# Kernel tuning notes

Measured on AMD Instinct MI355X. Metric: run time of the kernel, lower is better.

The kernel has to match this reference:

```python
import jax, jax.numpy as jnp
import numpy as np

B, S, D, H = 4, 2048, 1024, 16
HD = D // H  # 64
EPS = 1e-6


def _layernorm(x, scale, bias):
    mu = jnp.mean(x, axis=-1, keepdims=True)
    var = jnp.mean(jnp.square(x - mu), axis=-1, keepdims=True)
    return (x - mu) * jax.lax.rsqrt(var + EPS) * scale + bias


def setup_inputs() -> dict:
    key = jax.random.key(0)
    ks = jax.random.split(key, 10)
    s = 0.02
    return {
        "x": jax.random.normal(ks[0], (B, S, D), jnp.float32),
        "attention_mask": jnp.ones((B, 1, S, S), jnp.bool_),
        "eval": 1,
        "Wq": jax.random.normal(ks[1], (D, D), jnp.float32) * s,
        "bq": jnp.zeros((D,), jnp.float32),
        "Wk": jax.random.normal(ks[2], (D, D), jnp.float32) * s,
        "bk": jnp.zeros((D,), jnp.float32),
        "Wv": jax.random.normal(ks[3], (D, D), jnp.float32) * s,
        "bv": jnp.zeros((D,), jnp.float32),
        "Wo": jax.random.normal(ks[4], (D, D), jnp.float32) * s,
        "bo": jnp.zeros((D,), jnp.float32),
        "W1": jax.random.normal(ks[5], (D, D), jnp.float32) * s,
        "b1": jnp.zeros((D,), jnp.float32),
        "W2": jax.random.normal(ks[6], (D, D), jnp.float32) * s,
        "b2": jnp.zeros((D,), jnp.float32),
        "ln1_scale": jnp.ones((D,), jnp.float32),
        "ln1_bias": jnp.zeros((D,), jnp.float32),
        "ln2_scale": jnp.ones((D,), jnp.float32),
        "ln2_bias": jnp.zeros((D,), jnp.float32),
    }


def reference(x, attention_mask, eval, Wq, bq, Wk, bk, Wv, bv, Wo, bo,
              W1, b1, W2, b2, ln1_scale, ln1_bias, ln2_scale, ln2_bias):
    # --- MultiHeadAttention ---
    q = (x @ Wq + bq).reshape(B, S, H, HD)
    k = (x @ Wk + bk).reshape(B, S, H, HD)
    v = (x @ Wv + bv).reshape(B, S, H, HD)
    scores = jnp.einsum('bqhd,bkhd->bhqk', q, k) / jnp.sqrt(jnp.float32(HD))
    scores = jnp.where(attention_mask, scores, -jnp.inf)
    attn = jax.nn.softmax(scores, axis=-1)
    vals = jnp.einsum('bhqk,bkhd->bqhd', attn, v).reshape(B, S, D)
    attn_out = vals @ Wo + bo
    # --- residual + LN ---
    h = _layernorm(x + attn_out, ln1_scale, ln1_bias)
    # --- FeedForward (dropout deterministic -> identity) ---
    ff = jnp.maximum(h @ W1 + b1, 0.0) @ W2 + b2
    return _layernorm(h + ff, ln2_scale, ln2_bias)
```

## Files before the change

### kernel.cpp

```cpp
#include <hip/hip_runtime.h>

typedef __bf16 bf16;
typedef __bf16 bf16x8 __attribute__((ext_vector_type(8)));
typedef __bf16 bf16x4 __attribute__((ext_vector_type(4)));
typedef float f32x4 __attribute__((ext_vector_type(4)));
typedef float f32x16 __attribute__((ext_vector_type(16)));
typedef unsigned int uint;

#define BB 4
#define SS 2048
#define DD 1024
#define HH 16
#define HD 64
#define GM 8192
#define GN 1024
#define GK 1024
#define KVB 64
#define NT (SS / KVB)

__device__ __forceinline__ f32x4 mfma16(bf16x8 a, bf16x8 b, f32x4 c) {
    return __builtin_amdgcn_mfma_f32_16x16x32_bf16(a, b, c, 0, 0, 0);
}
__device__ __forceinline__ f32x16 mfma32(bf16x8 a, bf16x8 b, f32x16 c) {
    return __builtin_amdgcn_mfma_f32_32x32x16_bf16(a, b, c, 0, 0, 0);
}
__device__ __forceinline__ uint pack2(float x, float y) {
    union { bf16 b[2]; uint u; } uu;
    uu.b[0] = (bf16)x; uu.b[1] = (bf16)y;
    return uu.u;
}
__device__ __forceinline__ void gload16(const bf16* g, char* l) {
    __builtin_amdgcn_global_load_lds((const __attribute__((address_space(1))) void*)g,
                                     (__attribute__((address_space(3))) void*)l, 16, 0, 0);
}

__global__ __launch_bounds__(256) void cvt_kernel(const float* __restrict__ in, bf16* __restrict__ out, int n4) {
    int i = blockIdx.x * 256 + threadIdx.x;
    if (i < n4) {
        float4 v = *(const float4*)(in + (size_t)i * 4);
        bf16x4 o = {(bf16)v.x, (bf16)v.y, (bf16)v.z, (bf16)v.w};
        *(bf16x4*)(out + (size_t)i * 4) = o;
    }
}

__global__ __launch_bounds__(256) void wtrans6_kernel(const float* __restrict__ Wa, const float* __restrict__ Wb,
                                                      const float* __restrict__ Wc, const float* __restrict__ Wd,
                                                      const float* __restrict__ We, const float* __restrict__ Wf,
                                                      bf16* __restrict__ WtBase) {
    __shared__ float tile[64][65];
    const int t = threadIdx.x;
    const int z = blockIdx.z;
    const float* W = (z == 0) ? Wa : (z == 1) ? Wb : (z == 2) ? Wc : (z == 3) ? Wd : (z == 4) ? We : Wf;
    bf16* Wt = WtBase + ((size_t)z << 20);
    const int k0 = blockIdx.x * 64, n0 = blockIdx.y * 64;
#pragma unroll
    for (int i = 0; i < 16; ++i) {
        int idx = i * 256 + t;
        int r = idx >> 6, c = idx & 63;
        tile[r][c] = W[(size_t)(k0 + r) * DD + n0 + c];
    }
    __syncthreads();
#pragma unroll
    for (int i = 0; i < 16; ++i) {
        int idx = i * 256 + t;
        int r = idx >> 6, c = idx & 63;
        Wt[(size_t)(n0 + r) * DD + k0 + c] = (bf16)tile[c][r];
    }
}

__global__ __launch_bounds__(256) void vtrans_kernel(const bf16* __restrict__ V, bf16* __restrict__ Vt) {
    __shared__ bf16 tile[64][72];
    const int t = threadIdx.x;
    const int bh = blockIdx.y;
    const int b = bh >> 4, h = bh & 15;
    const int s0 = blockIdx.x * 64;
#pragma unroll
    for (int i = 0; i < 16; ++i) {
        int idx = i * 256 + t;
        int r = idx >> 6, c = idx & 63;
        tile[r][c] = V[(size_t)(b * SS + s0 + r) * DD + h * HD + c];
    }
    __syncthreads();
#pragma unroll
    for (int i = 0; i < 16; ++i) {
        int idx = i * 256 + t;
        int r = idx >> 6, c = idx & 63;
        Vt[((size_t)bh * HD + r) * SS + s0 + c] = tile[c][r];
    }
}

#define STAGE(buf, kt) { const int off_ = (kt) * 32; \
    gload16(pa + off_, lpa + (buf) * 16384); \
    gload16(pb + off_, lpb + (buf) * 16384); }

#define WAITB(n) { asm volatile("s_waitcnt vmcnt(" #n ")" ::: "memory"); \
    __builtin_amdgcn_s_barrier(); \
    __builtin_amdgcn_sched_barrier(0); }

#define KSTEP(c) { \
    const char* Asc_ = smem + (c) * 16384; \
    const char* Bsc_ = Asc_ + 8192; \
    bf16x8 af[2], bfr[4]; \
    _Pragma("unroll") for (int mi = 0; mi < 2; ++mi) \
        af[mi] = *(const bf16x8*)(Asc_ + (wr * 32 + mi * 16 + l16) * 64 + g * 16); \
    _Pragma("unroll") for (int ni = 0; ni < 4; ++ni) \
        bfr[ni] = *(const bf16x8*)(Bsc_ + (wc * 64 + ni * 16 + l16) * 64 + g * 16); \
    _Pragma("unroll") for (int mi = 0; mi < 2; ++mi) \
        _Pragma("unroll") for (int ni = 0; ni < 4; ++ni) \
            acc[mi][ni] = mfma16(af[mi], bfr[ni], acc[mi][ni]); }

template<int MODE>
__global__ __launch_bounds__(512) void gemm_bt(const bf16* __restrict__ A, const bf16* __restrict__ Bt,
                                               const float* __restrict__ bias0, const float* __restrict__ bias1,
                                               const float* __restrict__ bias2, const float* __restrict__ resid,
                                               void* __restrict__ C0, void* __restrict__ C1, void* __restrict__ C2) {
    const int gx = gridDim.x, gy = gridDim.y;
    const int wg = blockIdx.x + gx * blockIdx.y;
    const int xcd = wg & 7, j = wg >> 3;
    const int m_blk = xcd * (gx >> 3) + j / gy;
    const int n_blk = j % gy;
    const int m0 = m_blk * 128;
    const int n0 = n_blk * 128;
    const int t = threadIdx.x;
    const int l = t & 63, wid = t >> 6;
    const int l16 = l & 15, g = l >> 4;
    const int wr = wid >> 1, wc = wid & 1;

    __shared__ char smem[65536];

    const bf16* pa = A + (size_t)(m0 + (t >> 2)) * GK + (t & 3) * 8;
    const bf16* pb = Bt + (size_t)(n0 + (t >> 2)) * GK + (t & 3) * 8;
    char* lpa = smem + t * 16;
    char* lpb = smem + 8192 + t * 16;

    f32x4 z = {0.f, 0.f, 0.f, 0.f};
    f32x4 acc[2][4];
#pragma unroll
    for (int mi = 0; mi < 2; ++mi)
#pragma unroll
        for (int ni = 0; ni < 4; ++ni) acc[mi][ni] = z;

    STAGE(0, 0) STAGE(1, 1) STAGE(2, 2)

    for (int kb = 0; kb < 28; kb += 4) {
        WAITB(4) STAGE(3, kb + 3) KSTEP(0)
        WAITB(4) STAGE(0, kb + 4) KSTEP(1)
        WAITB(4) STAGE(1, kb + 5) KSTEP(2)
        WAITB(4) STAGE(2, kb + 6) KSTEP(3)
    }
    WAITB(4) STAGE(3, 31) KSTEP(0)
    WAITB(4) KSTEP(1)
    WAITB(2) KSTEP(2)
    WAITB(0) KSTEP(3)

    const int creg = (MODE == 0) ? (n0 >> 10) : 0;
    const float* bias = (creg == 0) ? bias0 : (creg == 1) ? bias1 : bias2;
    bf16* outb = (bf16*)((creg == 0) ? C0 : (creg == 1) ? C1 : C2);
    float* outf = (float*)C0;
    const int ncol0 = (MODE == 0) ? (n0 & 1023) : n0;
#pragma unroll
    for (int ni = 0; ni < 4; ++ni) {
        const int col = ncol0 + wc * 64 + ni * 16 + l16;
        const float bv = bias[col];
#pragma unroll
        for (int mi = 0; mi < 2; ++mi) {
            const int row0 = m0 + wr * 32 + mi * 16 + g * 4;
#pragma unroll
            for (int j2 = 0; j2 < 4; ++j2) {
                float v = acc[mi][ni][j2] + bv;
                if (MODE == 2) v = fmaxf(v, 0.f);
                if (MODE == 1) {
                    v += resid[(size_t)(row0 + j2) * GN + col];
                    outf[(size_t)(row0 + j2) * GN + col] = v;
                } else {
                    outb[(size_t)(row0 + j2) * GN + col] = (bf16)v;
                }
            }
        }
    }
}

#define PFRAG(P, OFF, DST) { \
    uint a0 = pack2(P[OFF + 0], P[OFF + 1]); \
    uint a1 = pack2(P[OFF + 2], P[OFF + 3]); \
    uint a2 = pack2(P[OFF + 4], P[OFF + 5]); \
    uint a3 = pack2(P[OFF + 6], P[OFF + 7]); \
    uint s0 = (uint)__shfl_xor((int)a0, 32); \
    uint s1 = (uint)__shfl_xor((int)a1, 32); \
    uint s2 = (uint)__shfl_xor((int)a2, 32); \
    uint s3 = (uint)__shfl_xor((int)a3, 32); \
    union { uint u[4]; bf16x8 v; } uu; \
    uu.u[0] = lh ? s2 : a0; \
    uu.u[1] = lh ? s3 : a1; \
    uu.u[2] = lh ? a2 : s0; \
    uu.u[3] = lh ? a3 : s1; \
    DST = uu.v; }

__global__ __launch_bounds__(512) void attn_kernel(const bf16* __restrict__ Q, const bf16* __restrict__ K,
                                                   const bf16* __restrict__ Vt, bf16* __restrict__ vals) {
    const int wg = blockIdx.x;
    const int bh = wg >> 3;
    const int b = bh >> 4, h = bh & 15;
    const int q0 = (wg & 7) << 8;
    const int t = threadIdx.x;
    const int w = t >> 6, l = t & 63;
    const int l31 = l & 31, lh = l >> 5;
    const int qrow = q0 + w * 32 + l31;

    __shared__ int4 lds4[2048];
    char* lds = (char*)lds4;

    const float QS = 0.125f * 1.44269504f;
    const bf16* qp = Q + ((size_t)(b * SS + qrow)) * DD + h * HD + lh * 8;
    bf16x8 qf[4];
#pragma unroll
    for (int dc = 0; dc < 4; ++dc) {
        bf16x8 v = *(const bf16x8*)(qp + dc * 16);
#pragma unroll
        for (int j = 0; j < 8; ++j) v[j] = (bf16)((float)v[j] * QS);
        qf[dc] = v;
    }

    const int srow = t >> 3, schunk = t & 7;
    const bf16* kgp = K + ((size_t)(b * SS + srow)) * DD + h * HD + schunk * 8;
    const bf16* vgp = Vt + ((size_t)(bh * HD + srow)) * SS + schunk * 8;
    const int soff = srow * 128 + ((schunk * 16) ^ ((srow & 7) << 4));

    int4 rk = *(const int4*)kgp;
    int4 rv = *(const int4*)vgp;
    *(int4*)(lds + soff) = rk;
    *(int4*)(lds + 8192 + soff) = rv;

    const int sw = (l & 7) << 4;
    f32x16 o0, o1;
#pragma unroll
    for (int i = 0; i < 16; ++i) { o0[i] = 0.f; o1[i] = 0.f; }
    float l_run = 0.f;
    __syncthreads();

    for (int kt = 0; kt < NT; ++kt) {
        const int cur = (kt & 1) << 14;
        if (kt + 1 < NT) {
            rk = *(const int4*)(kgp + (size_t)(kt + 1) * KVB * DD);
            rv = *(const int4*)(vgp + (kt + 1) * KVB);
        }
        const char* kb = lds + cur;
        const char* vb = kb + 8192;
        f32x16 st0, st1;
#pragma unroll
        for (int i = 0; i < 16; ++i) { st0[i] = 0.f; st1[i] = 0.f; }
        __builtin_amdgcn_s_setprio(1);
#pragma unroll
        for (int dc = 0; dc < 4; ++dc) {
            const int cb = (dc * 32 + lh * 16) ^ sw;
            bf16x8 ka0 = *(const bf16x8*)(kb + l31 * 128 + cb);
            bf16x8 ka1 = *(const bf16x8*)(kb + (32 + l31) * 128 + cb);
            st0 = mfma32(ka0, qf[dc], st0);
            st1 = mfma32(ka1, qf[dc], st1);
        }
        __builtin_amdgcn_s_setprio(0);
        float sum = 0.f;
#pragma unroll
        for (int i = 0; i < 16; ++i) { st0[i] = __builtin_amdgcn_exp2f(st0[i]); sum += st0[i]; }
#pragma unroll
        for (int i = 0; i < 16; ++i) { st1[i] = __builtin_amdgcn_exp2f(st1[i]); sum += st1[i]; }
        sum += __shfl_xor(sum, 32);
        l_run += sum;
        bf16x8 pf0, pf1, pf2, pf3;
        PFRAG(st0, 0, pf0); PFRAG(st0, 8, pf1); PFRAG(st1, 0, pf2); PFRAG(st1, 8, pf3);
        __builtin_amdgcn_s_setprio(1);
#pragma unroll
        for (int dt = 0; dt < 2; ++dt) {
            const int rb = (dt * 32 + l31) * 128;
            f32x16 acc = dt ? o1 : o0;
            acc = mfma32(*(const bf16x8*)(vb + rb + ((0 * 32 + lh * 16) ^ sw)), pf0, acc);
            acc = mfma32(*(const bf16x8*)(vb + rb + ((1 * 32 + lh * 16) ^ sw)), pf1, acc);
            acc = mfma32(*(const bf16x8*)(vb + rb + ((2 * 32 + lh * 16) ^ sw)), pf2, acc);
            acc = mfma32(*(const bf16x8*)(vb + rb + ((3 * 32 + lh * 16) ^ sw)), pf3, acc);
            if (dt) o1 = acc; else o0 = acc;
        }
        __builtin_amdgcn_s_setprio(0);
        if (kt + 1 < NT) {
            const int nxt = (~kt & 1) << 14;
            *(int4*)(lds + nxt + soff) = rk;
            *(int4*)(lds + nxt + 8192 + soff) = rv;
        }
        __syncthreads();
    }
    const float invl = 1.f / l_run;
    bf16* vp = vals + ((size_t)(b * SS + qrow)) * DD + h * HD;
#pragma unroll
    for (int dt = 0; dt < 2; ++dt) {
        const f32x16 oo = dt ? o1 : o0;
#pragma unroll
        for (int rg = 0; rg < 4; ++rg) {
            bf16x4 ov;
#pragma unroll
            for (int j = 0; j < 4; ++j) ov[j] = (bf16)(oo[rg * 4 + j] * invl);
            *(bf16x4*)(vp + dt * 32 + rg * 8 + lh * 4) = ov;
        }
    }
}

template<bool WB>
__global__ __launch_bounds__(256) void ln_kernel(const float* __restrict__ in,
                                                 const float* __restrict__ scale, const float* __restrict__ bias,
                                                 float* __restrict__ outf, bf16* __restrict__ outb) {
    const int row = blockIdx.x;
    const int t = threadIdx.x;
    const size_t base = (size_t)row * DD + t * 4;
    const float4 va = *(const float4*)(in + base);
    const float r0 = va.x, r1 = va.y, r2 = va.z, r3 = va.w;
    float s = r0 + r1 + r2 + r3;
    float q = r0 * r0 + r1 * r1 + r2 * r2 + r3 * r3;
#pragma unroll
    for (int d = 1; d < 64; d <<= 1) { s += __shfl_xor(s, d); q += __shfl_xor(q, d); }
    __shared__ float ss[4], qq[4];
    const int wid = t >> 6, l = t & 63;
    if (l == 0) { ss[wid] = s; qq[wid] = q; }
    __syncthreads();
    s = ss[0] + ss[1] + ss[2] + ss[3];
    q = qq[0] + qq[1] + qq[2] + qq[3];
    const float mean = s * (1.f / 1024.f);
    const float var = q * (1.f / 1024.f) - mean * mean;
    const float rstd = rsqrtf(var + 1e-6f);
    const float4 sc = *(const float4*)(scale + t * 4);
    const float4 bi = *(const float4*)(bias + t * 4);
    const float y0 = (r0 - mean) * rstd * sc.x + bi.x;
    const float y1 = (r1 - mean) * rstd * sc.y + bi.y;
    const float y2 = (r2 - mean) * rstd * sc.z + bi.z;
    const float y3 = (r3 - mean) * rstd * sc.w + bi.w;
    float4 yo; yo.x = y0; yo.y = y1; yo.z = y2; yo.w = y3;
    *(float4*)(outf + base) = yo;
    if (WB) {
        bf16x4 ob = {(bf16)y0, (bf16)y1, (bf16)y2, (bf16)y3};
        *(bf16x4*)(outb + base) = ob;
    }
}

extern "C" void kernel_launch(void* const* d_in, const int* in_sizes, int n_in,
                              void* d_out, int out_size, void* d_ws, size_t ws_size,
                              hipStream_t stream) {
    const float* x   = (const float*)d_in[0];
    const float* Wq  = (const float*)d_in[3];  const float* bq = (const float*)d_in[4];
    const float* Wk  = (const float*)d_in[5];  const float* bk = (const float*)d_in[6];
    const float* Wv  = (const float*)d_in[7];  const float* bv = (const float*)d_in[8];
    const float* Wo  = (const float*)d_in[9];  const float* bo = (const float*)d_in[10];
    const float* W1  = (const float*)d_in[11]; const float* b1 = (const float*)d_in[12];
    const float* W2  = (const float*)d_in[13]; const float* b2 = (const float*)d_in[14];
    const float* l1s = (const float*)d_in[15]; const float* l1b = (const float*)d_in[16];
    const float* l2s = (const float*)d_in[17]; const float* l2b = (const float*)d_in[18];

    char* ws = (char*)d_ws;
    bf16* WTq = (bf16*)ws;
    bf16* WTo = WTq + 3 * (1 << 20);
    bf16* WT1 = WTq + 4 * (1 << 20);
    bf16* WT2 = WTq + 5 * (1 << 20);
    char* A1 = ws + 12582912;
    char* A2 = A1 + 16777216;
    char* A3 = A2 + 16777216;
    char* A4 = A3 + 16777216;
    char* A5 = A4 + 16777216;

    bf16*  xb      = (bf16*)A1;
    bf16*  Qb      = (bf16*)A2;
    bf16*  Kb      = (bf16*)A3;
    bf16*  Vb      = (bf16*)A4;
    bf16*  Vt      = (bf16*)A5;
    bf16*  valsb   = (bf16*)A4;
    float* attnout = (float*)A2;
    float* h       = (float*)A5;
    bf16*  hb      = (bf16*)A4;
    bf16*  ff1b    = (bf16*)A1;
    float* ff2     = (float*)A2;
    float* out     = (float*)d_out;

    const dim3 blk(256);
    const dim3 gblk(512);

    wtrans6_kernel<<<dim3(16, 16, 6), blk, 0, stream>>>(Wq, Wk, Wv, Wo, W1, W2, WTq);
    cvt_kernel<<<8192, blk, 0, stream>>>(x, xb, GM * DD / 4);
    gemm_bt<0><<<dim3(GM / 128, 24), gblk, 0, stream>>>(xb, WTq, bq, bk, bv, nullptr, Qb, Kb, Vb);
    vtrans_kernel<<<dim3(SS / 64, BB * HH), blk, 0, stream>>>(Vb, Vt);
    attn_kernel<<<BB * HH * (SS / 256), 512, 0, stream>>>(Qb, Kb, Vt, valsb);
    gemm_bt<1><<<dim3(GM / 128, 8), gblk, 0, stream>>>(valsb, WTo, bo, bo, bo, x, attnout, nullptr, nullptr);
    ln_kernel<true><<<GM, blk, 0, stream>>>(attnout, l1s, l1b, h, hb);
    gemm_bt<2><<<dim3(GM / 128, 8), gblk, 0, stream>>>(hb, WT1, b1, b1, b1, nullptr, ff1b, nullptr, nullptr);
    gemm_bt<1><<<dim3(GM / 128, 8), gblk, 0, stream>>>(ff1b, WT2, b2, b2, b2, h, ff2, nullptr, nullptr);
    ln_kernel<false><<<GM, blk, 0, stream>>>(ff2, l2s, l2b, out, nullptr);
}
```

Measured before the change: 425.2 us.

## Rework GEMM to 256 threads with 32x32 MFMA, XOR-swizzled LDS and 3-stage pipeline

The GEMM kernel now uses 4 waves per 128x128 tile instead of 8. Each wave computes a 64x64 sub-tile with 32x32x16 bf16 MFMAs in place of 16x16x32. LDS rows are XOR-swizzled by chunk to cut bank conflicts, and the pipeline depth drops from four buffers to three so shared memory shrinks to 48KB. The aim is higher MFMA density and register reuse per wave, at the cost of fewer waves per block to hide latency and more loads issued per thread.

```diff
diff --git a/kernel.cpp b/kernel.cpp
--- a/kernel.cpp
+++ b/kernel.cpp
@@ -91,7 +91,9 @@
 
 #define STAGE(buf, kt) { const int off_ = (kt) * 32; \
     gload16(pa + off_, lpa + (buf) * 16384); \
-    gload16(pb + off_, lpb + (buf) * 16384); }
+    gload16(pa + 64 * GK + off_, lpa + (buf) * 16384 + 4096); \
+    gload16(pb + off_, lpb + (buf) * 16384); \
+    gload16(pb + 64 * GK + off_, lpb + (buf) * 16384 + 4096); }
 
 #define WAITB(n) { asm volatile("s_waitcnt vmcnt(" #n ")" ::: "memory"); \
     __builtin_amdgcn_s_barrier(); \
@@ -100,17 +102,18 @@
 #define KSTEP(c) { \
     const char* Asc_ = smem + (c) * 16384; \
     const char* Bsc_ = Asc_ + 8192; \
-    bf16x8 af[2], bfr[4]; \
+    bf16x8 af[2][2], bfr[2][2]; \
     _Pragma("unroll") for (int mi = 0; mi < 2; ++mi) \
-        af[mi] = *(const bf16x8*)(Asc_ + (wr * 32 + mi * 16 + l16) * 64 + g * 16); \
-    _Pragma("unroll") for (int ni = 0; ni < 4; ++ni) \
-        bfr[ni] = *(const bf16x8*)(Bsc_ + (wc * 64 + ni * 16 + l16) * 64 + g * 16); \
+      _Pragma("unroll") for (int ks = 0; ks < 2; ++ks) { \
+        af[mi][ks]  = *(const bf16x8*)(Asc_ + (wr * 64 + mi * 32 + l31) * 64 + ((ks * 32 + lh * 16) ^ sw4)); \
+        bfr[mi][ks] = *(const bf16x8*)(Bsc_ + (wc * 64 + mi * 32 + l31) * 64 + ((ks * 32 + lh * 16) ^ sw4)); } \
     _Pragma("unroll") for (int mi = 0; mi < 2; ++mi) \
-        _Pragma("unroll") for (int ni = 0; ni < 4; ++ni) \
-            acc[mi][ni] = mfma16(af[mi], bfr[ni], acc[mi][ni]); }
+      _Pragma("unroll") for (int ni = 0; ni < 2; ++ni) { \
+        acc[mi][ni] = mfma32(af[mi][0], bfr[ni][0], acc[mi][ni]); \
+        acc[mi][ni] = mfma32(af[mi][1], bfr[ni][1], acc[mi][ni]); } }
 
 template<int MODE>
-__global__ __launch_bounds__(512) void gemm_bt(const bf16* __restrict__ A, const bf16* __restrict__ Bt,
+__global__ __launch_bounds__(256) void gemm_bt(const bf16* __restrict__ A, const bf16* __restrict__ Bt,
                                                const float* __restrict__ bias0, const float* __restrict__ bias1,
                                                const float* __restrict__ bias2, const float* __restrict__ resid,
                                                void* __restrict__ C0, void* __restrict__ C1, void* __restrict__ C2) {
@@ -123,35 +126,39 @@
     const int n0 = n_blk * 128;
     const int t = threadIdx.x;
     const int l = t & 63, wid = t >> 6;
-    const int l16 = l & 15, g = l >> 4;
+    const int l31 = l & 31, lh = l >> 5;
+    const int sw4 = (l31 & 3) << 4;
     const int wr = wid >> 1, wc = wid & 1;
 
-    __shared__ char smem[65536];
-
-    const bf16* pa = A + (size_t)(m0 + (t >> 2)) * GK + (t & 3) * 8;
-    const bf16* pb = Bt + (size_t)(n0 + (t >> 2)) * GK + (t & 3) * 8;
+    __shared__ char smem[49152];
+
+    const int srow = t >> 2;
+    const int schk = (t & 3) ^ (srow & 3);
+    const bf16* pa = A + (size_t)(m0 + srow) * GK + schk * 8;
+    const bf16* pb = Bt + (size_t)(n0 + srow) * GK + schk * 8;
     char* lpa = smem + t * 16;
     char* lpb = smem + 8192 + t * 16;
 
-    f32x4 z = {0.f, 0.f, 0.f, 0.f};
-    f32x4 acc[2][4];
+    f32x16 acc[2][2];
 #pragma unroll
     for (int mi = 0; mi < 2; ++mi)
 #pragma unroll
-        for (int ni = 0; ni < 4; ++ni) acc[mi][ni] = z;
-
-    STAGE(0, 0) STAGE(1, 1) STAGE(2, 2)
-
-    for (int kb = 0; kb < 28; kb += 4) {
-        WAITB(4) STAGE(3, kb + 3) KSTEP(0)
-        WAITB(4) STAGE(0, kb + 4) KSTEP(1)
-        WAITB(4) STAGE(1, kb + 5) KSTEP(2)
-        WAITB(4) STAGE(2, kb + 6) KSTEP(3)
-    }
-    WAITB(4) STAGE(3, 31) KSTEP(0)
-    WAITB(4) KSTEP(1)
-    WAITB(2) KSTEP(2)
-    WAITB(0) KSTEP(3)
+        for (int ni = 0; ni < 2; ++ni)
+#pragma unroll
+            for (int i = 0; i < 16; ++i) acc[mi][ni][i] = 0.f;
+
+    STAGE(0, 0) STAGE(1, 1)
+
+    for (int kb = 0; kb < 27; kb += 3) {
+        WAITB(4) STAGE(2, kb + 2) KSTEP(0)
+        WAITB(4) STAGE(0, kb + 3) KSTEP(1)
+        WAITB(4) STAGE(1, kb + 4) KSTEP(2)
+    }
+    WAITB(4) STAGE(2, 29) KSTEP(0)
+    WAITB(4) STAGE(0, 30) KSTEP(1)
+    WAITB(4) STAGE(1, 31) KSTEP(2)
+    WAITB(4) KSTEP(0)
+    WAITB(0) KSTEP(1)
 
     const int creg = (MODE == 0) ? (n0 >> 10) : 0;
     const float* bias = (creg == 0) ? bias0 : (creg == 1) ? bias1 : bias2;
@@ -159,22 +166,23 @@
     float* outf = (float*)C0;
     const int ncol0 = (MODE == 0) ? (n0 & 1023) : n0;
 #pragma unroll
-    for (int ni = 0; ni < 4; ++ni) {
-        const int col = ncol0 + wc * 64 + ni * 16 + l16;
+    for (int mi = 0; mi < 2; ++mi)
+#pragma unroll
+    for (int ni = 0; ni < 2; ++ni) {
+        const int col = ncol0 + wc * 64 + ni * 32 + l31;
         const float bv = bias[col];
 #pragma unroll
-        for (int mi = 0; mi < 2; ++mi) {
-            const int row0 = m0 + wr * 32 + mi * 16 + g * 4;
-#pragma unroll
-            for (int j2 = 0; j2 < 4; ++j2) {
-                float v = acc[mi][ni][j2] + bv;
-                if (MODE == 2) v = fmaxf(v, 0.f);
-                if (MODE == 1) {
-                    v += resid[(size_t)(row0 + j2) * GN + col];
-                    outf[(size_t)(row0 + j2) * GN + col] = v;
-                } else {
-                    outb[(size_t)(row0 + j2) * GN + col] = (bf16)v;
-                }
+        for (int rg = 0; rg < 4; ++rg)
+#pragma unroll
+        for (int rr = 0; rr < 4; ++rr) {
+            const int row = m0 + wr * 64 + mi * 32 + rg * 8 + lh * 4 + rr;
+            float v = acc[mi][ni][rg * 4 + rr] + bv;
+            if (MODE == 2) v = fmaxf(v, 0.f);
+            if (MODE == 1) {
+                v += resid[(size_t)row * GN + col];
+                outf[(size_t)row * GN + col] = v;
+            } else {
+                outb[(size_t)row * GN + col] = (bf16)v;
             }
         }
     }
@@ -376,16 +384,15 @@
     float* out     = (float*)d_out;
 
     const dim3 blk(256);
-    const dim3 gblk(512);
 
     wtrans6_kernel<<<dim3(16, 16, 6), blk, 0, stream>>>(Wq, Wk, Wv, Wo, W1, W2, WTq);
     cvt_kernel<<<8192, blk, 0, stream>>>(x, xb, GM * DD / 4);
-    gemm_bt<0><<<dim3(GM / 128, 24), gblk, 0, stream>>>(xb, WTq, bq, bk, bv, nullptr, Qb, Kb, Vb);
+    gemm_bt<0><<<dim3(GM / 128, 24), blk, 0, stream>>>(xb, WTq, bq, bk, bv, nullptr, Qb, Kb, Vb);
     vtrans_kernel<<<dim3(SS / 64, BB * HH), blk, 0, stream>>>(Vb, Vt);
     attn_kernel<<<BB * HH * (SS / 256), 512, 0, stream>>>(Qb, Kb, Vt, valsb);
-    gemm_bt<1><<<dim3(GM / 128, 8), gblk, 0, stream>>>(valsb, WTo, bo, bo, bo, x, attnout, nullptr, nullptr);
+    gemm_bt<1><<<dim3(GM / 128, 8), blk, 0, stream>>>(valsb, WTo, bo, bo, bo, x, attnout, nullptr, nullptr);
     ln_kernel<true><<<GM, blk, 0, stream>>>(attnout, l1s, l1b, h, hb);
-    gemm_bt<2><<<dim3(GM / 128, 8), gblk, 0, stream>>>(hb, WT1, b1, b1, b1, nullptr, ff1b, nullptr, nullptr);
-    gemm_bt<1><<<dim3(GM / 128, 8), gblk, 0, stream>>>(ff1b, WT2, b2, b2, b2, h, ff2, nullptr, nullptr);
+    gemm_bt<2><<<dim3(GM / 128, 8), blk, 0, stream>>>(hb, WT1, b1, b1, b1, nullptr, ff1b, nullptr, nullptr);
+    gemm_bt<1><<<dim3(GM / 128, 8), blk, 0, stream>>>(ff1b, WT2, b2, b2, b2, h, ff2, nullptr, nullptr);
     ln_kernel<false><<<GM, blk, 0, stream>>>(ff2, l2s, l2b, out, nullptr);
 }
```

After: 427.6 us. Within noise of the previous version (+0.6%).
